# Performance work log

Hardware: AMD Instinct MI355X
Metric: run time of the kernel (lower is better)

The kernel has to match this reference:

```python
import jax, jax.numpy as jnp
import numpy as np

NUM_HEADS = 32
NUM_KV_HEADS = 8
HEAD_DIM = 64
HIDDEN = 2048
EPS = 1e-05
ROPE_THETA = 1000000.0


def _rmsnorm(x, w):
    # x: [..., head_dim]
    var = jnp.mean(x * x, axis=-1, keepdims=True)
    return w * (x * jax.lax.rsqrt(var + EPS))


def _rope(q, k):
    # q,k: [B, h, T, d]
    T, d = q.shape[2], q.shape[3]
    inv_freq = 1.0 / (ROPE_THETA ** (jnp.arange(0, d, 2, dtype=jnp.float32) / d))
    t = jnp.arange(T, dtype=jnp.float32)
    freqs = jnp.outer(t, inv_freq)               # [T, d/2]
    emb = jnp.concatenate([freqs, freqs], -1)    # [T, d]
    cos = jnp.cos(emb)[None, None].astype(q.dtype)
    sin = jnp.sin(emb)[None, None].astype(q.dtype)

    def rotate(x):
        x1, x2 = x[..., : d // 2], x[..., d // 2 :]
        return jnp.concatenate([-x2, x1], -1)

    return q * cos + rotate(q) * sin, k * cos + rotate(k) * sin


def setup_inputs() -> dict:
    key = jax.random.key(0)
    ks = jax.random.split(key, 7)
    s = 0.02
    x = jax.random.normal(ks[0], (2, 2048, HIDDEN), jnp.float32)
    Wq = jax.random.normal(ks[1], (HIDDEN, NUM_HEADS * HEAD_DIM), jnp.float32) * s
    Wk = jax.random.normal(ks[2], (HIDDEN, NUM_KV_HEADS * HEAD_DIM), jnp.float32) * s
    Wv = jax.random.normal(ks[3], (HIDDEN, NUM_KV_HEADS * HEAD_DIM), jnp.float32) * s
    Wo = jax.random.normal(ks[4], (NUM_HEADS * HEAD_DIM, HIDDEN), jnp.float32) * s
    q_ln_w = jnp.ones((HEAD_DIM,), jnp.float32)
    k_ln_w = jnp.ones((HEAD_DIM,), jnp.float32)
    return {"x": x, "Wq": Wq, "Wk": Wk, "Wv": Wv, "Wo": Wo, "q_ln_w": q_ln_w, "k_ln_w": k_ln_w}


def reference(x, Wq, Wk, Wv, Wo, q_ln_w, k_ln_w):
    B, T, _ = x.shape
    g = NUM_HEADS // NUM_KV_HEADS  # GQA groups = 4
    q = (x @ Wq).reshape(B, T, NUM_HEADS, HEAD_DIM)
    k = (x @ Wk).reshape(B, T, NUM_KV_HEADS, HEAD_DIM)
    v = (x @ Wv).reshape(B, T, NUM_KV_HEADS, HEAD_DIM)
    q = _rmsnorm(q, q_ln_w)
    k = _rmsnorm(k, k_ln_w)
    q = q.transpose(0, 2, 1, 3)  # [B, nh, T, d]
    k = k.transpose(0, 2, 1, 3)  # [B, nkv, T, d]
    v = v.transpose(0, 2, 1, 3)
    q, k = _rope(q, k)
    # native GQA: fold query heads into (kv_head, group) without repeating K/V
    qg = q.reshape(B, NUM_KV_HEADS, g, T, HEAD_DIM)
    scale = 1.0 / jnp.sqrt(jnp.array(HEAD_DIM, q.dtype))
    scores = jnp.einsum("bkgtd,bksd->bkgts", qg, k) * scale  # [B,nkv,g,T,T]
    causal = jnp.tril(jnp.ones((T, T), bool))
    scores = jnp.where(causal, scores, jnp.finfo(scores.dtype).min)
    probs = jax.nn.softmax(scores, axis=-1)
    out = jnp.einsum("bkgts,bksd->bkgtd", probs, v)  # [B,nkv,g,T,d]
    out = out.reshape(B, NUM_HEADS, T, HEAD_DIM).transpose(0, 2, 1, 3).reshape(B, T, -1)
    return out @ Wo
```

## Files before the change

### kernel.cpp

```cpp
#include <hip/hip_runtime.h>
#include <cstdint>
#include <cstddef>

typedef unsigned short u16;
typedef __attribute__((ext_vector_type(8))) short short8;
typedef __attribute__((ext_vector_type(4))) short short4v;
typedef __attribute__((ext_vector_type(4))) float float4v;
typedef __attribute__((ext_vector_type(4))) unsigned short ushort4v;
typedef __attribute__((ext_vector_type(2))) float float2v;

__device__ __forceinline__ u16 f2bf(float f) {
    union { float f; uint32_t u; } x; x.f = f;
    uint32_t r = x.u + 0x7fffu + ((x.u >> 16) & 1u);
    return (u16)(r >> 16);
}
__device__ __forceinline__ float bf2f(u16 b) {
    union { uint32_t u; float f; } x; x.u = ((uint32_t)b) << 16;
    return x.f;
}
__device__ __forceinline__ uint32_t pack_bf16x2(float lo, float hi) {
    union { float f; uint32_t u; } a, b; a.f = lo; b.f = hi;
    return __builtin_amdgcn_perm(b.u + 0x8000u, a.u + 0x8000u, 0x07060302u);
}
__device__ __forceinline__ void gload_lds16(const u16* g, u16* l) {
    __builtin_amdgcn_global_load_lds(
        (const __attribute__((address_space(1))) void*)g,
        (__attribute__((address_space(3))) void*)l,
        16, 0, 0);
}

__global__ __launch_bounds__(256) void cast_x(const float4v* __restrict__ x,
                                              ushort4v* __restrict__ xb, int n4) {
    int i = blockIdx.x * 256 + threadIdx.x;
    if (i >= n4) return;
    float4v v = x[i];
    ushort4v o;
    #pragma unroll
    for (int j = 0; j < 4; ++j) o[j] = f2bf(v[j]);
    xb[i] = o;
}

__global__ __launch_bounds__(256) void transpose_cast(const float* __restrict__ src,
                                                      u16* __restrict__ dst, int Ns) {
    __shared__ float lds[32][33];
    const int tid = threadIdx.x;
    const int n0 = blockIdx.x * 32;
    const int k0 = blockIdx.y * 32;
    const int row = tid >> 3;
    const int c4  = (tid & 7) * 4;
    const float4v v = *(const float4v*)(src + (size_t)(k0 + row) * Ns + n0 + c4);
    #pragma unroll
    for (int i = 0; i < 4; ++i) lds[row][c4 + i] = v[i];
    __syncthreads();
    const int nrow = tid >> 3;
    const int k4   = (tid & 7) * 4;
    ushort4v o;
    #pragma unroll
    for (int i = 0; i < 4; ++i) o[i] = f2bf(lds[k4 + i][nrow]);
    *(ushort4v*)(dst + (size_t)(n0 + nrow) * 2048 + k0 + k4) = o;
}

template<int WRITE_BF16>
__global__ __launch_bounds__(256) void gemm_bt(const u16* __restrict__ A,
                                               const u16* __restrict__ Bt,
                                               void* __restrict__ Cv,
                                               int M, int N, int K) {
    __shared__ u16 lds_a[128 * 32];
    __shared__ u16 lds_b[128 * 32];
    const int tid  = threadIdx.x;
    const int wave = tid >> 6;
    const int lane = tid & 63;
    const int quad = lane >> 4;
    const int l15  = lane & 15;
    const long m0 = (long)blockIdx.x * 128;
    const long n0 = (long)blockIdx.y * 128;
    const int wm = (wave >> 1) * 64;
    const int wn = (wave & 1) * 64;
    const int sa_row = lane >> 2;
    const int sa_col = (lane & 3) * 8;

    float4v acc[4][4];
    #pragma unroll
    for (int i = 0; i < 4; ++i)
        #pragma unroll
        for (int j = 0; j < 4; ++j)
            #pragma unroll
            for (int r = 0; r < 4; ++r) acc[i][j][r] = 0.0f;

    for (int k0 = 0; k0 < K; k0 += 32) {
        #pragma unroll
        for (int i = 0; i < 2; ++i) {
            const int slot = wave * 2 + i;
            const u16* ga = A  + (m0 + slot * 16 + sa_row) * (long)K + k0 + sa_col;
            gload_lds16(ga, lds_a + slot * 512);
            const u16* gb = Bt + (n0 + slot * 16 + sa_row) * (long)K + k0 + sa_col;
            gload_lds16(gb, lds_b + slot * 512);
        }
        __syncthreads();
        short8 af[4], bfr[4];
        #pragma unroll
        for (int mt = 0; mt < 4; ++mt)
            af[mt] = *(const short8*)(lds_a + (wm + mt * 16 + l15) * 32 + quad * 8);
        #pragma unroll
        for (int nt = 0; nt < 4; ++nt)
            bfr[nt] = *(const short8*)(lds_b + (wn + nt * 16 + l15) * 32 + quad * 8);
        #pragma unroll
        for (int mt = 0; mt < 4; ++mt)
            #pragma unroll
            for (int nt = 0; nt < 4; ++nt)
                acc[mt][nt] = __builtin_amdgcn_mfma_f32_16x16x32_bf16(af[mt], bfr[nt], acc[mt][nt], 0, 0, 0);
        __syncthreads();
    }
    #pragma unroll
    for (int mt = 0; mt < 4; ++mt) {
        #pragma unroll
        for (int nt = 0; nt < 4; ++nt) {
            const long gr = m0 + wm + mt * 16 + quad * 4;
            const long gc = n0 + wn + nt * 16 + l15;
            #pragma unroll
            for (int r = 0; r < 4; ++r) {
                const float v = acc[mt][nt][r];
                if (WRITE_BF16) ((u16*)Cv)[(gr + r) * N + gc] = f2bf(v);
                else            ((float*)Cv)[(gr + r) * N + gc] = v;
            }
        }
    }
}

__global__ __launch_bounds__(256) void rope_table(float2v* __restrict__ tab) {
    const int idx = blockIdx.x * 256 + threadIdx.x;
    const int t = idx >> 5;
    const int i = idx & 31;
    const float invf = exp2f(-(float)i * (19.931568569324174f / 32.0f));
    float sv, cv;
    sincosf((float)t * invf, &sv, &cv);
    float2v o; o[0] = cv; o[1] = sv;
    tab[idx] = o;
}

__global__ __launch_bounds__(256) void norm_rope(const u16* __restrict__ qkv,
                                                 const float* __restrict__ qw,
                                                 const float* __restrict__ kw,
                                                 const float2v* __restrict__ tab,
                                                 u16* __restrict__ Qr, u16* __restrict__ Kr) {
    const int W = blockIdx.x * 4 + (threadIdx.x >> 6);
    const int lane = threadIdx.x & 63;
    const int token = W / 40;
    const int u = W - token * 40;
    const int b = token >> 11;
    const int t = token & 2047;
    const bool isQ = (u < 32);
    const int col = isQ ? (u * 64 + lane) : (2048 + (u - 32) * 64 + lane);
    const float v = bf2f(qkv[(size_t)token * 3072 + col]);
    float ss = v * v;
    #pragma unroll
    for (int m = 1; m < 64; m <<= 1) ss += __shfl_xor(ss, m);
    const float rms = rsqrtf(ss * (1.0f / 64.0f) + 1e-5f);
    const float w = isQ ? qw[lane] : kw[lane];
    const float vn = v * rms * w;
    const float partner = __shfl_xor(vn, 32);
    const float2v cs = tab[t * 32 + (lane & 31)];
    float outv = vn * cs[0] + ((lane < 32) ? -partner : partner) * cs[1];
    if (isQ) {
        outv *= 0.18033688011112042f;
        Qr[(((size_t)b * 32 + u) * 2048 + t) * 64 + lane] = f2bf(outv);
    } else {
        Kr[(((size_t)b * 8 + (u - 32)) * 2048 + t) * 64 + lane] = f2bf(outv);
    }
}

__global__ __launch_bounds__(256) void v_transpose(const u16* __restrict__ qkv,
                                                   u16* __restrict__ Vr) {
    __shared__ u16 lds[32][36];
    const int tid = threadIdx.x;
    const int t0 = blockIdx.x * 32;
    const int d0 = blockIdx.y * 32;
    const int head = blockIdx.z;
    const int b = head >> 3, kh = head & 7;
    const int row = tid >> 3;
    const int c4  = (tid & 7) * 4;
    ushort4v val = *(const ushort4v*)(qkv + (size_t)(b * 2048 + t0 + row) * 3072
                                          + 2560 + kh * 64 + d0 + c4);
    #pragma unroll
    for (int i = 0; i < 4; ++i) lds[row][c4 + i] = val[i];
    __syncthreads();
    const int drow = tid >> 3;
    const int t4   = (tid & 7) * 4;
    ushort4v o;
    #pragma unroll
    for (int i = 0; i < 4; ++i) o[i] = lds[t4 + i][drow];
    *(ushort4v*)(Vr + ((size_t)head * 64 + d0 + drow) * 2048 + t0 + t4) = o;
}

#define KSTR 72
#define VSTR 136
__global__ __launch_bounds__(512, 4) void attn_fwd(const u16* __restrict__ Qr,
                                                   const u16* __restrict__ Kr,
                                                   const u16* __restrict__ Vt,
                                                   u16* __restrict__ Ob) {
    __shared__ u16 lds_k[2][128 * KSTR];
    __shared__ u16 lds_vt[2][64 * VSTR];
    const int tid  = threadIdx.x;
    const int wave = tid >> 6;
    const int lane = tid & 63;
    const int quad = lane >> 4;
    const int l15  = lane & 15;
    const int qxB = blockIdx.x;
    const int qxA = 15 - qxB;
    const int bh = blockIdx.y;
    const int b = bh >> 5, h = bh & 31;
    const int kh = h >> 2;
    const u16* Qh = Qr + ((size_t)(b * 32 + h))  * 2048 * 64;
    const u16* Kh = Kr + ((size_t)(b * 8 + kh))  * 2048 * 64;
    const u16* Vh = Vt + ((size_t)(b * 8 + kh))  * 64 * 2048;

    const int k_key0 = tid >> 3;
    const int k_d0   = (tid & 7) * 8;
    const int v_d0   = tid >> 4;
    const int v_k8   = (tid & 15) * 8;

    const int qrowA = qxA * 128 + wave * 16 + l15;
    const int qrowB = qxB * 128 + wave * 16 + l15;
    short8 qfA[2], qfB[2];
    #pragma unroll
    for (int ks = 0; ks < 2; ++ks) {
        qfA[ks] = *(const short8*)(Qh + (size_t)qrowA * 64 + ks * 32 + quad * 8);
        qfB[ks] = *(const short8*)(Qh + (size_t)qrowB * 64 + ks * 32 + quad * 8);
    }
    short8 qf0 = qfA[0], qf1 = qfA[1];
    int qrow_cur = qrowA;

    float m_i = -3e38f, l_i = 0.0f;
    float4v Oacc[4];
    #pragma unroll
    for (int dt = 0; dt < 4; ++dt)
        #pragma unroll
        for (int r = 0; r < 4; ++r) Oacc[dt][r] = 0.0f;

    short8 kreg[2], vreg[2];
    #pragma unroll
    for (int i = 0; i < 2; ++i) {
        kreg[i] = *(const short8*)(Kh + (size_t)(k_key0 + i * 64) * 64 + k_d0);
        vreg[i] = *(const short8*)(Vh + (size_t)(v_d0 + i * 32) * 2048 + v_k8);
    }
    #pragma unroll
    for (int i = 0; i < 2; ++i) {
        *(short8*)(lds_k[0]  + (k_key0 + i * 64) * KSTR + k_d0) = kreg[i];
        *(short8*)(lds_vt[0] + (v_d0 + i * 32) * VSTR + v_k8)   = vreg[i];
    }
    __syncthreads();

    const int n_it = 17;
    for (int i = 0; i < n_it; ++i) {
        const int p = i & 1;
        const bool last = (i == n_it - 1);
        const int kt_cur = (i <= qxA) ? i : (i - qxA - 1);
        const int kt0 = kt_cur << 7;

        if (!last) {
            const int ip1 = i + 1;
            const int ktn = (ip1 <= qxA) ? ip1 : (ip1 - qxA - 1);
            const size_t nk0 = (size_t)(ktn << 7);
            #pragma unroll
            for (int j = 0; j < 2; ++j) {
                kreg[j] = *(const short8*)(Kh + (nk0 + k_key0 + j * 64) * 64 + k_d0);
                vreg[j] = *(const short8*)(Vh + (size_t)(v_d0 + j * 32) * 2048 + nk0 + v_k8);
            }
        }

        float4v S[8];
        #pragma unroll
        for (int nt = 0; nt < 8; ++nt)
            #pragma unroll
            for (int r = 0; r < 4; ++r) S[nt][r] = 0.0f;
        #pragma unroll
        for (int ks = 0; ks < 2; ++ks) {
            const short8 qf = ks ? qf1 : qf0;
            #pragma unroll
            for (int nt = 0; nt < 8; ++nt) {
                short8 kf = *(const short8*)(lds_k[p] + (nt * 16 + l15) * KSTR + ks * 32 + quad * 8);
                S[nt] = __builtin_amdgcn_mfma_f32_16x16x32_bf16(kf, qf, S[nt], 0, 0, 0);
            }
        }
        if (i == qxA || last) {
            #pragma unroll
            for (int nt = 0; nt < 8; ++nt) {
                const int keyb = kt0 + nt * 16 + quad * 4;
                #pragma unroll
                for (int r = 0; r < 4; ++r)
                    if (keyb + r > qrow_cur) S[nt][r] = -3e38f;
            }
        }
        float mx = S[0][0];
        #pragma unroll
        for (int nt = 0; nt < 8; ++nt)
            #pragma unroll
            for (int r = 0; r < 4; ++r) mx = fmaxf(mx, S[nt][r]);
        mx = fmaxf(mx, __shfl_xor(mx, 16));
        mx = fmaxf(mx, __shfl_xor(mx, 32));
        const float mnew = fmaxf(m_i, mx);
        const float alpha = __builtin_amdgcn_exp2f(m_i - mnew);
        m_i = mnew;
        float rs = 0.0f;
        #pragma unroll
        for (int nt = 0; nt < 8; ++nt)
            #pragma unroll
            for (int r = 0; r < 4; ++r) {
                const float pv = __builtin_amdgcn_exp2f(S[nt][r] - mnew);
                S[nt][r] = pv;
                rs += pv;
            }
        rs += __shfl_xor(rs, 16);
        rs += __shfl_xor(rs, 32);
        l_i = l_i * alpha + rs;
        #pragma unroll
        for (int dt = 0; dt < 4; ++dt)
            #pragma unroll
            for (int r = 0; r < 4; ++r) Oacc[dt][r] *= alpha;

        #pragma unroll
        for (int nt = 0; nt < 8; ++nt) {
            union { uint32_t u[2]; short4v s; } pu;
            pu.u[0] = pack_bf16x2(S[nt][0], S[nt][1]);
            pu.u[1] = pack_bf16x2(S[nt][2], S[nt][3]);
            const short4v pf = pu.s;
            #pragma unroll
            for (int dt = 0; dt < 4; ++dt) {
                const short4v vf = *(const short4v*)(lds_vt[p] + (dt * 16 + l15) * VSTR + nt * 16 + quad * 4);
                Oacc[dt] = __builtin_amdgcn_mfma_f32_16x16x16bf16_1k(vf, pf, Oacc[dt], 0, 0, 0);
            }
        }

        if (i == qxA) {
            const float rl = 1.0f / l_i;
            #pragma unroll
            for (int dt = 0; dt < 4; ++dt) {
                ushort4v o;
                #pragma unroll
                for (int r = 0; r < 4; ++r) o[r] = f2bf(Oacc[dt][r] * rl);
                *(ushort4v*)(Ob + ((size_t)(b * 2048 + qrowA)) * 2048 + h * 64 + dt * 16 + quad * 4) = o;
            }
            m_i = -3e38f;
            l_i = 0.0f;
            qf0 = qfB[0];
            qf1 = qfB[1];
            qrow_cur = qrowB;
        }

        if (!last) {
            #pragma unroll
            for (int j = 0; j < 2; ++j) {
                *(short8*)(lds_k[1 - p]  + (k_key0 + j * 64) * KSTR + k_d0) = kreg[j];
                *(short8*)(lds_vt[1 - p] + (v_d0 + j * 32) * VSTR + v_k8)   = vreg[j];
            }
        }
        __syncthreads();
    }
    const float rl = 1.0f / l_i;
    #pragma unroll
    for (int dt = 0; dt < 4; ++dt) {
        ushort4v o;
        #pragma unroll
        for (int r = 0; r < 4; ++r) o[r] = f2bf(Oacc[dt][r] * rl);
        *(ushort4v*)(Ob + ((size_t)(b * 2048 + qrowB)) * 2048 + h * 64 + dt * 16 + quad * 4) = o;
    }
}

extern "C" void kernel_launch(void* const* d_in, const int* in_sizes, int n_in,
                              void* d_out, int out_size, void* d_ws, size_t ws_size,
                              hipStream_t stream) {
    (void)in_sizes; (void)n_in; (void)out_size; (void)ws_size;
    const float* x  = (const float*)d_in[0];
    const float* Wq = (const float*)d_in[1];
    const float* Wk = (const float*)d_in[2];
    const float* Wv = (const float*)d_in[3];
    const float* Wo = (const float*)d_in[4];
    const float* qw = (const float*)d_in[5];
    const float* kw = (const float*)d_in[6];
    float* out = (float*)d_out;

    char* ws = (char*)d_ws;
    size_t off = 0;
    auto alloc = [&](size_t bytes) {
        char* p = ws + off;
        off += (bytes + 255) & ~(size_t)255;
        return p;
    };
    u16* xb     = (u16*)alloc((size_t)8388608 * 2);
    u16* wqkv_t = (u16*)alloc((size_t)3072 * 2048 * 2);
    u16* wo_t   = (u16*)alloc((size_t)2048 * 2048 * 2);
    u16* qkv    = (u16*)alloc((size_t)4096 * 3072 * 2);
    u16* q_r    = (u16*)alloc((size_t)2 * 32 * 2048 * 64 * 2);
    u16* k_r    = (u16*)alloc((size_t)2 * 8 * 2048 * 64 * 2);
    u16* v_r    = (u16*)alloc((size_t)2 * 8 * 64 * 2048 * 2);
    float2v* rtab = (float2v*)alloc((size_t)2048 * 32 * 8);
    u16* attnb  = xb;

    hipLaunchKernelGGL(cast_x, dim3(8192), dim3(256), 0, stream,
                       (const float4v*)x, (ushort4v*)xb, 2097152);
    hipLaunchKernelGGL(rope_table, dim3(256), dim3(256), 0, stream, rtab);
    hipLaunchKernelGGL(transpose_cast, dim3(64, 64), dim3(256), 0, stream, Wq, wqkv_t, 2048);
    hipLaunchKernelGGL(transpose_cast, dim3(16, 64), dim3(256), 0, stream, Wk, wqkv_t + (size_t)2048 * 2048, 512);
    hipLaunchKernelGGL(transpose_cast, dim3(16, 64), dim3(256), 0, stream, Wv, wqkv_t + (size_t)2560 * 2048, 512);
    hipLaunchKernelGGL(transpose_cast, dim3(64, 64), dim3(256), 0, stream, Wo, wo_t, 2048);
    hipLaunchKernelGGL(HIP_KERNEL_NAME(gemm_bt<1>), dim3(32, 24), dim3(256), 0, stream,
                       xb, wqkv_t, (void*)qkv, 4096, 3072, 2048);
    hipLaunchKernelGGL(norm_rope, dim3(40960), dim3(256), 0, stream, qkv, qw, kw, rtab, q_r, k_r);
    hipLaunchKernelGGL(v_transpose, dim3(64, 2, 16), dim3(256), 0, stream, qkv, v_r);
    hipLaunchKernelGGL(attn_fwd, dim3(8, 64), dim3(512), 0, stream, q_r, k_r, v_r, attnb);
    hipLaunchKernelGGL(HIP_KERNEL_NAME(gemm_bt<0>), dim3(32, 16), dim3(256), 0, stream,
                       attnb, wo_t, (void*)out, 4096, 2048, 2048);
}
```

Before: 344.2 us.

## Fuse QK RMSNorm, RoPE and V transpose into QKV GEMM epilogue; merge prep kernels

Merges the x cast, RoPE table build and all four weight transpose-casts into one prep launch. The QKV GEMM epilogue now applies per-head RMSNorm (via lane shuffles across the 64-column wave tile) and RoPE, writing Q, K and transposed V directly. This removes the bf16 qkv intermediate round trip and the separate norm_rope and v_transpose launches. The epilogue stores are scattered 2-byte writes, and the bf16 rounding now happens after normalization rather than before it.

```diff
diff --git a/kernel.cpp b/kernel.cpp
--- a/kernel.cpp
+++ b/kernel.cpp
@@ -29,26 +29,59 @@
         16, 0, 0);
 }
 
-__global__ __launch_bounds__(256) void cast_x(const float4v* __restrict__ x,
-                                              ushort4v* __restrict__ xb, int n4) {
-    int i = blockIdx.x * 256 + threadIdx.x;
-    if (i >= n4) return;
-    float4v v = x[i];
-    ushort4v o;
-    #pragma unroll
-    for (int j = 0; j < 4; ++j) o[j] = f2bf(v[j]);
-    xb[i] = o;
-}
-
-__global__ __launch_bounds__(256) void transpose_cast(const float* __restrict__ src,
-                                                      u16* __restrict__ dst, int Ns) {
+__global__ __launch_bounds__(256) void prep(const float4v* __restrict__ x,
+                                            const float* __restrict__ Wq,
+                                            const float* __restrict__ Wk,
+                                            const float* __restrict__ Wv,
+                                            const float* __restrict__ Wo,
+                                            ushort4v* __restrict__ xb,
+                                            u16* __restrict__ wqkv_t,
+                                            u16* __restrict__ wo_t,
+                                            float2v* __restrict__ tab) {
     __shared__ float lds[32][33];
+    const int bid = blockIdx.x;
     const int tid = threadIdx.x;
-    const int n0 = blockIdx.x * 32;
-    const int k0 = blockIdx.y * 32;
+    if (bid < 8192) {
+        const int i = bid * 256 + tid;
+        float4v v = x[i];
+        ushort4v o;
+        #pragma unroll
+        for (int j = 0; j < 4; ++j) o[j] = f2bf(v[j]);
+        xb[i] = o;
+        return;
+    }
+    if (bid < 8448) {
+        const int idx = (bid - 8192) * 256 + tid;
+        const int t = idx >> 5;
+        const int i = idx & 31;
+        const float invf = exp2f(-(float)i * (19.931568569324174f / 32.0f));
+        float sv, cv;
+        sincosf((float)t * invf, &sv, &cv);
+        float2v o; o[0] = cv; o[1] = sv;
+        tab[idx] = o;
+        return;
+    }
+    const float* src;
+    int Ns, n0, k0, scol0;
+    u16* dst;
+    if (bid < 14592) {
+        const int id = bid - 8448;
+        const int bx = id % 96, by = id / 96;
+        n0 = bx * 32; k0 = by * 32;
+        if (n0 < 2048)      { src = Wq; Ns = 2048; scol0 = n0; }
+        else if (n0 < 2560) { src = Wk; Ns = 512;  scol0 = n0 - 2048; }
+        else                { src = Wv; Ns = 512;  scol0 = n0 - 2560; }
+        dst = wqkv_t;
+    } else {
+        const int id = bid - 14592;
+        const int bx = id & 63, by = id >> 6;
+        n0 = bx * 32; k0 = by * 32;
+        src = Wo; Ns = 2048; scol0 = n0;
+        dst = wo_t;
+    }
     const int row = tid >> 3;
     const int c4  = (tid & 7) * 4;
-    const float4v v = *(const float4v*)(src + (size_t)(k0 + row) * Ns + n0 + c4);
+    const float4v v = *(const float4v*)(src + (size_t)(k0 + row) * Ns + scol0 + c4);
     #pragma unroll
     for (int i = 0; i < 4; ++i) lds[row][c4 + i] = v[i];
     __syncthreads();
@@ -60,10 +93,9 @@
     *(ushort4v*)(dst + (size_t)(n0 + nrow) * 2048 + k0 + k4) = o;
 }
 
-template<int WRITE_BF16>
 __global__ __launch_bounds__(256) void gemm_bt(const u16* __restrict__ A,
                                                const u16* __restrict__ Bt,
-                                               void* __restrict__ Cv,
+                                               float* __restrict__ C,
                                                int M, int N, int K) {
     __shared__ u16 lds_a[128 * 32];
     __shared__ u16 lds_b[128 * 32];
@@ -118,78 +150,127 @@
             const long gr = m0 + wm + mt * 16 + quad * 4;
             const long gc = n0 + wn + nt * 16 + l15;
             #pragma unroll
+            for (int r = 0; r < 4; ++r)
+                C[(gr + r) * N + gc] = acc[mt][nt][r];
+        }
+    }
+}
+
+__global__ __launch_bounds__(256) void gemm_qkv(const u16* __restrict__ A,
+                                                const u16* __restrict__ Bt,
+                                                const float* __restrict__ qw,
+                                                const float* __restrict__ kw,
+                                                const float2v* __restrict__ tab,
+                                                u16* __restrict__ Qr,
+                                                u16* __restrict__ Kr,
+                                                u16* __restrict__ Vt) {
+    const int K = 2048;
+    __shared__ u16 lds_a[128 * 32];
+    __shared__ u16 lds_b[128 * 32];
+    const int tid  = threadIdx.x;
+    const int wave = tid >> 6;
+    const int lane = tid & 63;
+    const int quad = lane >> 4;
+    const int l15  = lane & 15;
+    const long m0 = (long)blockIdx.x * 128;
+    const long n0 = (long)blockIdx.y * 128;
+    const int wm = (wave >> 1) * 64;
+    const int wn = (wave & 1) * 64;
+    const int sa_row = lane >> 2;
+    const int sa_col = (lane & 3) * 8;
+
+    float4v acc[4][4];
+    #pragma unroll
+    for (int i = 0; i < 4; ++i)
+        #pragma unroll
+        for (int j = 0; j < 4; ++j)
+            #pragma unroll
+            for (int r = 0; r < 4; ++r) acc[i][j][r] = 0.0f;
+
+    for (int k0 = 0; k0 < K; k0 += 32) {
+        #pragma unroll
+        for (int i = 0; i < 2; ++i) {
+            const int slot = wave * 2 + i;
+            const u16* ga = A  + (m0 + slot * 16 + sa_row) * (long)K + k0 + sa_col;
+            gload_lds16(ga, lds_a + slot * 512);
+            const u16* gb = Bt + (n0 + slot * 16 + sa_row) * (long)K + k0 + sa_col;
+            gload_lds16(gb, lds_b + slot * 512);
+        }
+        __syncthreads();
+        short8 af[4], bfr[4];
+        #pragma unroll
+        for (int mt = 0; mt < 4; ++mt)
+            af[mt] = *(const short8*)(lds_a + (wm + mt * 16 + l15) * 32 + quad * 8);
+        #pragma unroll
+        for (int nt = 0; nt < 4; ++nt)
+            bfr[nt] = *(const short8*)(lds_b + (wn + nt * 16 + l15) * 32 + quad * 8);
+        #pragma unroll
+        for (int mt = 0; mt < 4; ++mt)
+            #pragma unroll
+            for (int nt = 0; nt < 4; ++nt)
+                acc[mt][nt] = __builtin_amdgcn_mfma_f32_16x16x32_bf16(af[mt], bfr[nt], acc[mt][nt], 0, 0, 0);
+        __syncthreads();
+    }
+
+    const int col0 = (int)n0 + wn;
+    if (col0 < 2560) {
+        const bool isQ = (col0 < 2048);
+        const float* lw = isQ ? qw : kw;
+        float wreg[4];
+        #pragma unroll
+        for (int nt = 0; nt < 4; ++nt) wreg[nt] = lw[nt * 16 + l15];
+        const float qs = isQ ? 0.18033688011112042f : 1.0f;
+        u16* dst = isQ ? (Qr + ((size_t)(col0 >> 6)) * 2048 * 64)
+                       : (Kr + ((size_t)((col0 - 2048) >> 6)) * 2048 * 64);
+        const size_t head_stride = isQ ? ((size_t)32 * 2048 * 64) : ((size_t)8 * 2048 * 64);
+        #pragma unroll
+        for (int mt = 0; mt < 4; ++mt) {
+            const int gr0 = (int)m0 + wm + mt * 16 + quad * 4;
+            const int b = gr0 >> 11, tt0 = gr0 & 2047;
+            float rms[4];
+            #pragma unroll
             for (int r = 0; r < 4; ++r) {
-                const float v = acc[mt][nt][r];
-                if (WRITE_BF16) ((u16*)Cv)[(gr + r) * N + gc] = f2bf(v);
-                else            ((float*)Cv)[(gr + r) * N + gc] = v;
-            }
-        }
-    }
-}
-
-__global__ __launch_bounds__(256) void rope_table(float2v* __restrict__ tab) {
-    const int idx = blockIdx.x * 256 + threadIdx.x;
-    const int t = idx >> 5;
-    const int i = idx & 31;
-    const float invf = exp2f(-(float)i * (19.931568569324174f / 32.0f));
-    float sv, cv;
-    sincosf((float)t * invf, &sv, &cv);
-    float2v o; o[0] = cv; o[1] = sv;
-    tab[idx] = o;
-}
-
-__global__ __launch_bounds__(256) void norm_rope(const u16* __restrict__ qkv,
-                                                 const float* __restrict__ qw,
-                                                 const float* __restrict__ kw,
-                                                 const float2v* __restrict__ tab,
-                                                 u16* __restrict__ Qr, u16* __restrict__ Kr) {
-    const int W = blockIdx.x * 4 + (threadIdx.x >> 6);
-    const int lane = threadIdx.x & 63;
-    const int token = W / 40;
-    const int u = W - token * 40;
-    const int b = token >> 11;
-    const int t = token & 2047;
-    const bool isQ = (u < 32);
-    const int col = isQ ? (u * 64 + lane) : (2048 + (u - 32) * 64 + lane);
-    const float v = bf2f(qkv[(size_t)token * 3072 + col]);
-    float ss = v * v;
-    #pragma unroll
-    for (int m = 1; m < 64; m <<= 1) ss += __shfl_xor(ss, m);
-    const float rms = rsqrtf(ss * (1.0f / 64.0f) + 1e-5f);
-    const float w = isQ ? qw[lane] : kw[lane];
-    const float vn = v * rms * w;
-    const float partner = __shfl_xor(vn, 32);
-    const float2v cs = tab[t * 32 + (lane & 31)];
-    float outv = vn * cs[0] + ((lane < 32) ? -partner : partner) * cs[1];
-    if (isQ) {
-        outv *= 0.18033688011112042f;
-        Qr[(((size_t)b * 32 + u) * 2048 + t) * 64 + lane] = f2bf(outv);
+                float s = 0.0f;
+                #pragma unroll
+                for (int nt = 0; nt < 4; ++nt) s += acc[mt][nt][r] * acc[mt][nt][r];
+                s += __shfl_xor(s, 1);
+                s += __shfl_xor(s, 2);
+                s += __shfl_xor(s, 4);
+                s += __shfl_xor(s, 8);
+                rms[r] = rsqrtf(s * (1.0f / 64.0f) + 1e-5f);
+            }
+            u16* rowp = dst + (size_t)b * head_stride + (size_t)tt0 * 64;
+            #pragma unroll
+            for (int nt = 0; nt < 2; ++nt) {
+                const int i = nt * 16 + l15;
+                #pragma unroll
+                for (int r = 0; r < 4; ++r) {
+                    const float2v cs = tab[(tt0 + r) * 32 + i];
+                    const float v1 = acc[mt][nt][r]     * rms[r] * wreg[nt];
+                    const float v2 = acc[mt][nt + 2][r] * rms[r] * wreg[nt + 2];
+                    const float o1 = (v1 * cs[0] - v2 * cs[1]) * qs;
+                    const float o2 = (v2 * cs[0] + v1 * cs[1]) * qs;
+                    rowp[(size_t)r * 64 + i]      = f2bf(o1);
+                    rowp[(size_t)r * 64 + i + 32] = f2bf(o2);
+                }
+            }
+        }
     } else {
-        Kr[(((size_t)b * 8 + (u - 32)) * 2048 + t) * 64 + lane] = f2bf(outv);
-    }
-}
-
-__global__ __launch_bounds__(256) void v_transpose(const u16* __restrict__ qkv,
-                                                   u16* __restrict__ Vr) {
-    __shared__ u16 lds[32][36];
-    const int tid = threadIdx.x;
-    const int t0 = blockIdx.x * 32;
-    const int d0 = blockIdx.y * 32;
-    const int head = blockIdx.z;
-    const int b = head >> 3, kh = head & 7;
-    const int row = tid >> 3;
-    const int c4  = (tid & 7) * 4;
-    ushort4v val = *(const ushort4v*)(qkv + (size_t)(b * 2048 + t0 + row) * 3072
-                                          + 2560 + kh * 64 + d0 + c4);
-    #pragma unroll
-    for (int i = 0; i < 4; ++i) lds[row][c4 + i] = val[i];
-    __syncthreads();
-    const int drow = tid >> 3;
-    const int t4   = (tid & 7) * 4;
-    ushort4v o;
-    #pragma unroll
-    for (int i = 0; i < 4; ++i) o[i] = lds[t4 + i][drow];
-    *(ushort4v*)(Vr + ((size_t)head * 64 + d0 + drow) * 2048 + t0 + t4) = o;
+        const int kh = (col0 - 2560) >> 6;
+        #pragma unroll
+        for (int mt = 0; mt < 4; ++mt) {
+            const int gr0 = (int)m0 + wm + mt * 16 + quad * 4;
+            const int b = gr0 >> 11, tt0 = gr0 & 2047;
+            #pragma unroll
+            for (int nt = 0; nt < 4; ++nt) {
+                const int d = nt * 16 + l15;
+                ushort4v o;
+                #pragma unroll
+                for (int r = 0; r < 4; ++r) o[r] = f2bf(acc[mt][nt][r]);
+                *(ushort4v*)(Vt + (((size_t)(b * 8 + kh)) * 64 + d) * 2048 + tt0) = o;
+            }
+        }
+    }
 }
 
 #define KSTR 72
@@ -389,25 +470,18 @@
     u16* xb     = (u16*)alloc((size_t)8388608 * 2);
     u16* wqkv_t = (u16*)alloc((size_t)3072 * 2048 * 2);
     u16* wo_t   = (u16*)alloc((size_t)2048 * 2048 * 2);
-    u16* qkv    = (u16*)alloc((size_t)4096 * 3072 * 2);
     u16* q_r    = (u16*)alloc((size_t)2 * 32 * 2048 * 64 * 2);
     u16* k_r    = (u16*)alloc((size_t)2 * 8 * 2048 * 64 * 2);
     u16* v_r    = (u16*)alloc((size_t)2 * 8 * 64 * 2048 * 2);
     float2v* rtab = (float2v*)alloc((size_t)2048 * 32 * 8);
     u16* attnb  = xb;
 
-    hipLaunchKernelGGL(cast_x, dim3(8192), dim3(256), 0, stream,
-                       (const float4v*)x, (ushort4v*)xb, 2097152);
-    hipLaunchKernelGGL(rope_table, dim3(256), dim3(256), 0, stream, rtab);
-    hipLaunchKernelGGL(transpose_cast, dim3(64, 64), dim3(256), 0, stream, Wq, wqkv_t, 2048);
-    hipLaunchKernelGGL(transpose_cast, dim3(16, 64), dim3(256), 0, stream, Wk, wqkv_t + (size_t)2048 * 2048, 512);
-    hipLaunchKernelGGL(transpose_cast, dim3(16, 64), dim3(256), 0, stream, Wv, wqkv_t + (size_t)2560 * 2048, 512);
-    hipLaunchKernelGGL(transpose_cast, dim3(64, 64), dim3(256), 0, stream, Wo, wo_t, 2048);
-    hipLaunchKernelGGL(HIP_KERNEL_NAME(gemm_bt<1>), dim3(32, 24), dim3(256), 0, stream,
-                       xb, wqkv_t, (void*)qkv, 4096, 3072, 2048);
-    hipLaunchKernelGGL(norm_rope, dim3(40960), dim3(256), 0, stream, qkv, qw, kw, rtab, q_r, k_r);
-    hipLaunchKernelGGL(v_transpose, dim3(64, 2, 16), dim3(256), 0, stream, qkv, v_r);
+    hipLaunchKernelGGL(prep, dim3(18688), dim3(256), 0, stream,
+                       (const float4v*)x, Wq, Wk, Wv, Wo,
+                       (ushort4v*)xb, wqkv_t, wo_t, rtab);
+    hipLaunchKernelGGL(gemm_qkv, dim3(32, 24), dim3(256), 0, stream,
+                       xb, wqkv_t, qw, kw, rtab, q_r, k_r, v_r);
     hipLaunchKernelGGL(attn_fwd, dim3(8, 64), dim3(512), 0, stream, q_r, k_r, v_r, attnb);
-    hipLaunchKernelGGL(HIP_KERNEL_NAME(gemm_bt<0>), dim3(32, 16), dim3(256), 0, stream,
-                       attnb, wo_t, (void*)out, 4096, 2048, 2048);
-}
+    hipLaunchKernelGGL(gemm_bt, dim3(32, 16), dim3(256), 0, stream,
+                       attnb, wo_t, out, 4096, 2048, 2048);
+}
```

Result: faster. 331.1 us (-3.8%).
